# Performance work log

Measured on AMD Instinct MI355X. Metric: run time of the kernel, lower is better.

## Reference

```python
import jax, jax.numpy as jnp
import numpy as np

V = 50000   # vocab_size
D = 128     # emb_dim
HID = 64    # hidden_dim
HEADS = 4   # gat_heads
N = 20000   # n_nodes
E = 320000  # n_edges
SLOPE = 0.2 # PyG GATConv leaky_relu negative_slope


def setup_inputs() -> dict:
    key = jax.random.key(0)
    ks = jax.random.split(key, 13)
    nrm = lambda k, shp: jax.random.normal(k, shp, jnp.float32) * 0.1
    return {
        "node_idxs": jax.random.randint(ks[0], (N,), 0, V),
        "edge_index": jax.random.randint(ks[1], (2, E), 0, N),
        "emb": nrm(ks[2], (V, D)),
        # GAT layer 1: in=D, out=HID per head, HEADS heads, concat
        "W1": nrm(ks[3], (D, HEADS * HID)),
        "att_src1": nrm(ks[4], (HEADS, HID)),
        "att_dst1": nrm(ks[5], (HEADS, HID)),
        "b1": jnp.zeros((HEADS * HID,), jnp.float32),
        # GAT layer 2: in=HEADS*HID, out=HID, 1 head
        "W2": nrm(ks[6], (HEADS * HID, HID)),
        "att_src2": nrm(ks[7], (1, HID)),
        "att_dst2": nrm(ks[8], (1, HID)),
        "b2": jnp.zeros((HID,), jnp.float32),
        # attentional pooling gate MLP: Linear(HID,HID) -> ReLU -> Linear(HID,1)
        "gate_W1": nrm(ks[9], (HID, HID)),
        "gate_b1": jnp.zeros((HID,), jnp.float32),
        "gate_W2": nrm(ks[10], (HID, 1)),
        "gate_b2": jnp.zeros((1,), jnp.float32),
    }


def _segment_softmax(logits, seg, num_segments):
    # numerically stable softmax over edges grouped by destination node
    m = jax.ops.segment_max(logits, seg, num_segments=num_segments)
    e = jnp.exp(logits - m[seg])
    s = jax.ops.segment_sum(e, seg, num_segments=num_segments)
    return e / s[seg]


def _gat_layer(x, src, dst, n, W, a_src, a_dst, b, heads, ch):
    h = (x @ W).reshape(n, heads, ch)                 # [N,H,C]
    alpha_src = jnp.einsum('nhc,hc->nh', h, a_src)    # [N,H]
    alpha_dst = jnp.einsum('nhc,hc->nh', h, a_dst)    # [N,H]
    logits = jax.nn.leaky_relu(alpha_src[src] + alpha_dst[dst], SLOPE)  # [E,H]
    alpha = _segment_softmax(logits, dst, n)          # [E,H]
    out = jax.ops.segment_sum(h[src] * alpha[..., None], dst, num_segments=n)  # [N,H,C]
    return out.reshape(n, heads * ch) + b


def reference(node_idxs, edge_index, emb, W1, att_src1, att_dst1, b1,
              W2, att_src2, att_dst2, b2, gate_W1, gate_b1, gate_W2, gate_b2):
    n = node_idxs.shape[0]
    # PyG GATConv default add_self_loops=True
    loops = jnp.arange(n)
    src = jnp.concatenate([edge_index[0], loops])
    dst = jnp.concatenate([edge_index[1], loops])

    x = emb[node_idxs]                                                  # [N,D]
    x = jax.nn.elu(_gat_layer(x, src, dst, n, W1, att_src1, att_dst1, b1, HEADS, HID))
    x = jax.nn.elu(_gat_layer(x, src, dst, n, W2, att_src2, att_dst2, b2, 1, HID))

    # AttentionalAggregation with index=zeros -> global softmax-gated pool
    gate = jax.nn.relu(x @ gate_W1 + gate_b1) @ gate_W2 + gate_b2       # [N,1]
    w = jax.nn.softmax(gate, axis=0)
    return jnp.sum(w * x, axis=0, keepdims=True)                        # [1,HID]
```

## Files before the change

### kernel.cpp

```cpp
#include <hip/hip_runtime.h>

typedef float v4 __attribute__((ext_vector_type(4)));

__device__ __forceinline__ float leaky(float x) { return x >= 0.f ? x : 0.2f * x; }
__device__ __forceinline__ float elu(float x) { return x > 0.f ? x : expm1f(x); }

__global__ void k_deg(const int* __restrict__ ei, int* __restrict__ deg, int nE, int eT) {
  int e = blockIdx.x * blockDim.x + threadIdx.x;
  if (e >= eT) return;
  int d = (e < nE) ? ei[nE + e] : (e - nE);
  atomicAdd(&deg[d], 1);
}

__global__ void k_scan(const int* __restrict__ deg, int* __restrict__ rowptr,
                       int* __restrict__ cursor, int nN, int eT) {
  __shared__ int sd[1024];
  int t = threadIdx.x;
  int chunk = (nN + 1023) >> 10;
  int beg = t * chunk;
  int end = beg + chunk; if (end > nN) end = nN;
  int s = 0;
  for (int i = beg; i < end; ++i) s += deg[i];
  sd[t] = s;
  __syncthreads();
  for (int off = 1; off < 1024; off <<= 1) {
    int v = (t >= off) ? sd[t - off] : 0;
    __syncthreads();
    sd[t] += v;
    __syncthreads();
  }
  int run = sd[t] - s;
  for (int i = beg; i < end; ++i) { rowptr[i] = run; cursor[i] = run; run += deg[i]; }
  if (t == 0) rowptr[nN] = eT;
}

__global__ void k_scatter(const int* __restrict__ ei, int* __restrict__ cursor,
                          int* __restrict__ srt, int nE, int eT) {
  int e = blockIdx.x * blockDim.x + threadIdx.x;
  if (e >= eT) return;
  int s, d;
  if (e < nE) { s = ei[e]; d = ei[nE + e]; } else { s = d = e - nE; }
  int pos = atomicAdd(&cursor[d], 1);
  srt[pos] = s;
}

__global__ __launch_bounds__(256) void k_gemm1(
    const int* __restrict__ nidx, const float* __restrict__ emb,
    const float* __restrict__ W1, const float* __restrict__ asv,
    const float* __restrict__ adv, float* __restrict__ h1,
    float* __restrict__ as1, float* __restrict__ ad1, int nN) {
  __shared__ __align__(16) float xs[64 * 68];
  __shared__ __align__(16) float Ws[64 * 64];
  int t = threadIdx.x;
  int nbase = (blockIdx.x >> 2) * 64;
  int head  = blockIdx.x & 3;
  int cbase = head * 64;
  int c0 = (t & 15) * 4;
  int n0 = (t >> 4) * 4;
  float acc[4][4];
  for (int i = 0; i < 4; ++i) for (int j = 0; j < 4; ++j) acc[i][j] = 0.f;
  v4 z = (v4)(0.f);
  for (int kc = 0; kc < 2; ++kc) {
    __syncthreads();
    {
      int sn = t >> 2;
      int node = nbase + sn;
      int kp = (t & 3) * 16;
      bool v = node < nN;
      const float* sp = &emb[(size_t)nidx[v ? node : nN - 1] * 128 + kc * 64 + kp];
      v4 a0 = v ? *(const v4*)(sp + 0)  : z;
      v4 a1 = v ? *(const v4*)(sp + 4)  : z;
      v4 a2 = v ? *(const v4*)(sp + 8)  : z;
      v4 a3 = v ? *(const v4*)(sp + 12) : z;
      *(v4*)&xs[sn * 68 + kp + 0]  = a0;
      *(v4*)&xs[sn * 68 + kp + 4]  = a1;
      *(v4*)&xs[sn * 68 + kp + 8]  = a2;
      *(v4*)&xs[sn * 68 + kp + 12] = a3;
    }
    {
      int kk = t >> 2;
      int cp = (t & 3) * 16;
      const float* wp = &W1[(size_t)(kc * 64 + kk) * 256 + cbase + cp];
      v4 w0 = *(const v4*)(wp + 0);
      v4 w1 = *(const v4*)(wp + 4);
      v4 w2 = *(const v4*)(wp + 8);
      v4 w3 = *(const v4*)(wp + 12);
      *(v4*)&Ws[kk * 64 + cp + 0]  = w0;
      *(v4*)&Ws[kk * 64 + cp + 4]  = w1;
      *(v4*)&Ws[kk * 64 + cp + 8]  = w2;
      *(v4*)&Ws[kk * 64 + cp + 12] = w3;
    }
    __syncthreads();
    #pragma unroll 4
    for (int kk = 0; kk < 64; kk += 4) {
      v4 xv[4], wv[4];
      for (int i = 0; i < 4; ++i) xv[i] = *(const v4*)&xs[(n0 + i) * 68 + kk];
      for (int j = 0; j < 4; ++j) wv[j] = *(const v4*)&Ws[(kk + j) * 64 + c0];
      for (int i = 0; i < 4; ++i)
        for (int j = 0; j < 4; ++j) {
          float xd = xv[i][j];
          acc[i][0] += xd * wv[j][0];
          acc[i][1] += xd * wv[j][1];
          acc[i][2] += xd * wv[j][2];
          acc[i][3] += xd * wv[j][3];
        }
    }
  }
  v4 asl = *(const v4*)&asv[cbase + c0];
  v4 adl = *(const v4*)&adv[cbase + c0];
  for (int i = 0; i < 4; ++i) {
    int node = nbase + n0 + i;
    v4 o; o[0] = acc[i][0]; o[1] = acc[i][1]; o[2] = acc[i][2]; o[3] = acc[i][3];
    float ps = o[0]*asl[0] + o[1]*asl[1] + o[2]*asl[2] + o[3]*asl[3];
    float pd = o[0]*adl[0] + o[1]*adl[1] + o[2]*adl[2] + o[3]*adl[3];
    ps += __shfl_xor(ps, 1); pd += __shfl_xor(pd, 1);
    ps += __shfl_xor(ps, 2); pd += __shfl_xor(pd, 2);
    ps += __shfl_xor(ps, 4); pd += __shfl_xor(pd, 4);
    ps += __shfl_xor(ps, 8); pd += __shfl_xor(pd, 8);
    if (node < nN) {
      *(v4*)&h1[(size_t)node * 256 + cbase + c0] = o;
      if ((t & 15) == 0) {
        as1[(size_t)node * 4 + head] = ps;
        ad1[(size_t)node * 4 + head] = pd;
      }
    }
  }
}

__global__ __launch_bounds__(256) void k_agg1(
    const float* __restrict__ h1, const float* __restrict__ as1,
    const float* __restrict__ ad1, const float* __restrict__ b1,
    const int* __restrict__ rowptr, const int* __restrict__ srt,
    float* __restrict__ x2, int nN) {
  __shared__ int   ss[4][64];
  __shared__ float sw[4][256];
  int t = threadIdx.x;
  int wv = t >> 6, lane = t & 63;
  int n = blockIdx.x * 4 + wv;
  if (n >= nN) return;
  int ms0 = rowptr[n], ms1 = rowptr[n + 1];
  v4 adn = *(const v4*)&ad1[(size_t)n * 4];
  int h = lane >> 4;
  v4 acc = (v4)(0.f);
  float den = 0.f;
  for (int base = ms0; base < ms1; base += 64) {
    int m = ms1 - base; if (m > 64) m = 64;
    asm volatile("s_waitcnt lgkmcnt(0)" ::: "memory");
    __builtin_amdgcn_wave_barrier();
    if (lane < m) {
      int s = srt[base + lane];
      ss[wv][lane] = s;
      v4 a = *(const v4*)&as1[(size_t)s * 4];
      sw[wv][lane * 4 + 0] = __expf(leaky(a[0] + adn[0]));
      sw[wv][lane * 4 + 1] = __expf(leaky(a[1] + adn[1]));
      sw[wv][lane * 4 + 2] = __expf(leaky(a[2] + adn[2]));
      sw[wv][lane * 4 + 3] = __expf(leaky(a[3] + adn[3]));
    }
    asm volatile("s_waitcnt lgkmcnt(0)" ::: "memory");
    __builtin_amdgcn_wave_barrier();
    #pragma unroll 8
    for (int j = 0; j < m; ++j) {
      int s = ss[wv][j];
      float wj = sw[wv][j * 4 + h];
      v4 hv = *(const v4*)&h1[(size_t)s * 256 + lane * 4];
      acc[0] += wj * hv[0];
      acc[1] += wj * hv[1];
      acc[2] += wj * hv[2];
      acc[3] += wj * hv[3];
      den += wj;
    }
  }
  v4 bb = *(const v4*)&b1[lane * 4];
  float inv = 1.f / den;
  v4 o;
  o[0] = elu(acc[0] * inv + bb[0]);
  o[1] = elu(acc[1] * inv + bb[1]);
  o[2] = elu(acc[2] * inv + bb[2]);
  o[3] = elu(acc[3] * inv + bb[3]);
  *(v4*)&x2[(size_t)n * 256 + lane * 4] = o;
}

__global__ __launch_bounds__(256) void k_gemm2(
    const float* __restrict__ x2, const float* __restrict__ W2,
    const float* __restrict__ asv, const float* __restrict__ adv,
    float* __restrict__ h2, float* __restrict__ as2, float* __restrict__ ad2, int nN) {
  __shared__ __align__(16) float xs[32 * 68];
  __shared__ __align__(16) float Ws[64 * 64];
  int t = threadIdx.x;
  int nbase = blockIdx.x * 32;
  int c0 = (t & 15) * 4;
  int n0 = (t >> 4) * 2;
  float acc[2][4];
  for (int i = 0; i < 2; ++i) for (int j = 0; j < 4; ++j) acc[i][j] = 0.f;
  v4 z = (v4)(0.f);
  for (int kc = 0; kc < 4; ++kc) {
    __syncthreads();
    {
      int sn = t >> 3;
      int node = nbase + sn;
      int kp = (t & 7) * 8;
      bool v = node < nN;
      const float* sp = &x2[(size_t)(v ? node : nN - 1) * 256 + kc * 64 + kp];
      v4 a0 = v ? *(const v4*)(sp + 0) : z;
      v4 a1 = v ? *(const v4*)(sp + 4) : z;
      *(v4*)&xs[sn * 68 + kp + 0] = a0;
      *(v4*)&xs[sn * 68 + kp + 4] = a1;
    }
    {
      int kk = t >> 2;
      int cp = (t & 3) * 16;
      const float* wp = &W2[(size_t)(kc * 64 + kk) * 64 + cp];
      v4 w0 = *(const v4*)(wp + 0);
      v4 w1 = *(const v4*)(wp + 4);
      v4 w2 = *(const v4*)(wp + 8);
      v4 w3 = *(const v4*)(wp + 12);
      *(v4*)&Ws[kk * 64 + cp + 0]  = w0;
      *(v4*)&Ws[kk * 64 + cp + 4]  = w1;
      *(v4*)&Ws[kk * 64 + cp + 8]  = w2;
      *(v4*)&Ws[kk * 64 + cp + 12] = w3;
    }
    __syncthreads();
    #pragma unroll 4
    for (int kk = 0; kk < 64; kk += 4) {
      v4 xv[2], wv[4];
      for (int i = 0; i < 2; ++i) xv[i] = *(const v4*)&xs[(n0 + i) * 68 + kk];
      for (int j = 0; j < 4; ++j) wv[j] = *(const v4*)&Ws[(kk + j) * 64 + c0];
      for (int i = 0; i < 2; ++i)
        for (int j = 0; j < 4; ++j) {
          float xd = xv[i][j];
          acc[i][0] += xd * wv[j][0];
          acc[i][1] += xd * wv[j][1];
          acc[i][2] += xd * wv[j][2];
          acc[i][3] += xd * wv[j][3];
        }
    }
  }
  v4 asl = *(const v4*)&asv[c0];
  v4 adl = *(const v4*)&adv[c0];
  for (int i = 0; i < 2; ++i) {
    int node = nbase + n0 + i;
    v4 o; o[0] = acc[i][0]; o[1] = acc[i][1]; o[2] = acc[i][2]; o[3] = acc[i][3];
    float ps = o[0]*asl[0] + o[1]*asl[1] + o[2]*asl[2] + o[3]*asl[3];
    float pd = o[0]*adl[0] + o[1]*adl[1] + o[2]*adl[2] + o[3]*adl[3];
    ps += __shfl_xor(ps, 1); pd += __shfl_xor(pd, 1);
    ps += __shfl_xor(ps, 2); pd += __shfl_xor(pd, 2);
    ps += __shfl_xor(ps, 4); pd += __shfl_xor(pd, 4);
    ps += __shfl_xor(ps, 8); pd += __shfl_xor(pd, 8);
    if (node < nN) {
      *(v4*)&h2[(size_t)node * 64 + c0] = o;
      if ((t & 15) == 0) { as2[node] = ps; ad2[node] = pd; }
    }
  }
}

__global__ __launch_bounds__(256) void k_agg2(
    const float* __restrict__ h2, const float* __restrict__ as2,
    const float* __restrict__ ad2, const float* __restrict__ b2,
    const int* __restrict__ rowptr, const int* __restrict__ srt,
    float* __restrict__ x3, int nN) {
  __shared__ int   ss[4][64];
  __shared__ float sw[4][64];
  int t = threadIdx.x;
  int wv = t >> 6, lane = t & 63;
  int n = blockIdx.x * 4 + wv;
  if (n >= nN) return;
  int ms0 = rowptr[n], ms1 = rowptr[n + 1];
  float adn = ad2[n];
  float acc = 0.f, den = 0.f;
  for (int base = ms0; base < ms1; base += 64) {
    int m = ms1 - base; if (m > 64) m = 64;
    asm volatile("s_waitcnt lgkmcnt(0)" ::: "memory");
    __builtin_amdgcn_wave_barrier();
    if (lane < m) {
      int s = srt[base + lane];
      ss[wv][lane] = s;
      sw[wv][lane] = __expf(leaky(as2[s] + adn));
    }
    asm volatile("s_waitcnt lgkmcnt(0)" ::: "memory");
    __builtin_amdgcn_wave_barrier();
    #pragma unroll 8
    for (int j = 0; j < m; ++j) {
      int s = ss[wv][j];
      float wj = sw[wv][j];
      acc += wj * h2[(size_t)s * 64 + lane];
      den += wj;
    }
  }
  x3[(size_t)n * 64 + lane] = elu(acc / den + b2[lane]);
}

__global__ __launch_bounds__(512) void k_gatepool(
    const float* __restrict__ x3, const float* __restrict__ gW1,
    const float* __restrict__ gb1, const float* __restrict__ gW2,
    const float* __restrict__ gb2, float* __restrict__ pnum,
    float* __restrict__ pden, int nN) {
  __shared__ __align__(16) float gwT[64 * 68];
  __shared__ float xr[8][64];
  __shared__ float snum[8][64];
  __shared__ float sden[8];
  int t = threadIdx.x;
  int wv = t >> 6, lane = t & 63;
  for (int i = t; i < 4096; i += 512) {
    int d = i >> 6, c = i & 63;
    gwT[c * 68 + d] = gW1[i];
  }
  float gb1l = gb1[lane];
  float gw2l = gW2[lane];
  float gb2s = gb2[0];
  __syncthreads();
  float num = 0.f, den = 0.f;
  int nIt = (nN + 2047) >> 11;
  int off0 = blockIdx.x * 8 + wv;
  for (int it = 0; it < nIt; ++it) {
    int n = off0 + it * 2048;
    bool v = n < nN;
    float xv = v ? x3[(size_t)n * 64 + lane] : 0.f;
    xr[wv][lane] = xv;
    asm volatile("s_waitcnt lgkmcnt(0)" ::: "memory");
    __builtin_amdgcn_wave_barrier();
    float hid = gb1l;
    for (int d4 = 0; d4 < 64; d4 += 4) {
      v4 xs4 = *(const v4*)&xr[wv][d4];
      v4 gv  = *(const v4*)&gwT[lane * 68 + d4];
      hid += xs4[0] * gv[0] + xs4[1] * gv[1] + xs4[2] * gv[2] + xs4[3] * gv[3];
    }
    hid = fmaxf(hid, 0.f);
    float p = hid * gw2l;
    for (int o = 32; o; o >>= 1) p += __shfl_xor(p, o);
    float g = __expf(p + gb2s);
    if (v) { num += g * xv; den += g; }
    asm volatile("s_waitcnt lgkmcnt(0)" ::: "memory");
    __builtin_amdgcn_wave_barrier();
  }
  snum[wv][lane] = num;
  if (lane == 0) sden[wv] = den;
  __syncthreads();
  if (t < 64) {
    float s = 0.f;
    for (int k = 0; k < 8; ++k) s += snum[k][t];
    pnum[blockIdx.x * 64 + t] = s;
  }
  if (t == 0) {
    float s = 0.f;
    for (int k = 0; k < 8; ++k) s += sden[k];
    pden[blockIdx.x] = s;
  }
}

__global__ void k_final(const float* __restrict__ pnum, const float* __restrict__ pden,
                        float* __restrict__ out) {
  int t = threadIdx.x;
  float s = 0.f, dn = 0.f;
  for (int b = 0; b < 256; ++b) { s += pnum[b * 64 + t]; dn += pden[b]; }
  out[t] = s / dn;
}

extern "C" void kernel_launch(void* const* d_in, const int* in_sizes, int n_in,
                              void* d_out, int out_size, void* d_ws, size_t ws_size,
                              hipStream_t stream) {
  const int*   nidx = (const int*)d_in[0];
  const int*   ei   = (const int*)d_in[1];
  const float* emb  = (const float*)d_in[2];
  const float* W1   = (const float*)d_in[3];
  const float* as1v = (const float*)d_in[4];
  const float* ad1v = (const float*)d_in[5];
  const float* b1   = (const float*)d_in[6];
  const float* W2   = (const float*)d_in[7];
  const float* as2v = (const float*)d_in[8];
  const float* ad2v = (const float*)d_in[9];
  const float* b2   = (const float*)d_in[10];
  const float* gW1  = (const float*)d_in[11];
  const float* gb1  = (const float*)d_in[12];
  const float* gW2  = (const float*)d_in[13];
  const float* gb2  = (const float*)d_in[14];
  float* out = (float*)d_out;

  const int nN = in_sizes[0];
  const int nE = in_sizes[1] / 2;
  const int eT = nE + nN;

  float* f = (float*)d_ws;
  size_t off = 0;
  float* h1   = f + off; off += (size_t)nN * 256;
  float* x2   = f + off; off += (size_t)nN * 256;
  float* as1  = f + off; off += (size_t)nN * 4;
  float* ad1  = f + off; off += (size_t)nN * 4;
  float* as2  = f + off; off += nN;
  float* ad2  = f + off; off += nN;
  float* pnum = f + off; off += 256 * 64;
  float* pden = f + off; off += 256;
  int* deg    = (int*)(f + off); off += nN;
  int* rowptr = (int*)(f + off); off += nN + 1;
  int* cursor = (int*)(f + off); off += nN;
  int* srt    = (int*)(f + off); off += eT;

  float* h2 = h1;
  float* x3 = h1 + (size_t)nN * 128;

  hipMemsetAsync(deg, 0, (size_t)nN * sizeof(int), stream);

  int eb = (eT + 255) / 256;
  k_deg    <<<eb, 256, 0, stream>>>(ei, deg, nE, eT);
  k_scan   <<<1, 1024, 0, stream>>>(deg, rowptr, cursor, nN, eT);
  k_scatter<<<eb, 256, 0, stream>>>(ei, cursor, srt, nE, eT);

  int nt64 = (nN + 63) / 64;
  k_gemm1 <<<nt64 * 4, 256, 0, stream>>>(nidx, emb, W1, as1v, ad1v, h1, as1, ad1, nN);
  k_agg1  <<<(nN + 3) / 4, 256, 0, stream>>>(h1, as1, ad1, b1, rowptr, srt, x2, nN);

  k_gemm2 <<<(nN + 31) / 32, 256, 0, stream>>>(x2, W2, as2v, ad2v, h2, as2, ad2, nN);
  k_agg2  <<<(nN + 3) / 4, 256, 0, stream>>>(h2, as2, ad2, b2, rowptr, srt, x3, nN);

  k_gatepool<<<256, 512, 0, stream>>>(x3, gW1, gb1, gW2, gb2, pnum, pden, nN);
  k_final   <<<1, 64, 0, stream>>>(pnum, pden, out);
}
```

Baseline: 289.8 us.

## Fuse CSR build with GEMM1 tiles and fuse agg2 with gated pooling

The degree count and scan now run in one kernel alongside half of the GEMM1 tiles, with the last block doing the scan. The scatter runs in a second kernel alongside the other half of the tiles. Layer-2 aggregation is fused with the gate MLP and pooling, and the final division is done with atomics plus a last-block reduction. The goal is fewer launches, no x3 round trip through memory, and overlap of the graph preprocessing with GEMM work. In exchange it adds atomic float accumulation (nondeterministic order), a serial 256-thread scan, and a persistent tail grid of only 256 blocks, which may cut parallelism for the aggregation.

```diff
diff --git a/kernel.cpp b/kernel.cpp
--- a/kernel.cpp
+++ b/kernel.cpp
@@ -5,55 +5,16 @@
 __device__ __forceinline__ float leaky(float x) { return x >= 0.f ? x : 0.2f * x; }
 __device__ __forceinline__ float elu(float x) { return x > 0.f ? x : expm1f(x); }
 
-__global__ void k_deg(const int* __restrict__ ei, int* __restrict__ deg, int nE, int eT) {
-  int e = blockIdx.x * blockDim.x + threadIdx.x;
-  if (e >= eT) return;
-  int d = (e < nE) ? ei[nE + e] : (e - nE);
-  atomicAdd(&deg[d], 1);
-}
-
-__global__ void k_scan(const int* __restrict__ deg, int* __restrict__ rowptr,
-                       int* __restrict__ cursor, int nN, int eT) {
-  __shared__ int sd[1024];
-  int t = threadIdx.x;
-  int chunk = (nN + 1023) >> 10;
-  int beg = t * chunk;
-  int end = beg + chunk; if (end > nN) end = nN;
-  int s = 0;
-  for (int i = beg; i < end; ++i) s += deg[i];
-  sd[t] = s;
-  __syncthreads();
-  for (int off = 1; off < 1024; off <<= 1) {
-    int v = (t >= off) ? sd[t - off] : 0;
-    __syncthreads();
-    sd[t] += v;
-    __syncthreads();
-  }
-  int run = sd[t] - s;
-  for (int i = beg; i < end; ++i) { rowptr[i] = run; cursor[i] = run; run += deg[i]; }
-  if (t == 0) rowptr[nN] = eT;
-}
-
-__global__ void k_scatter(const int* __restrict__ ei, int* __restrict__ cursor,
-                          int* __restrict__ srt, int nE, int eT) {
-  int e = blockIdx.x * blockDim.x + threadIdx.x;
-  if (e >= eT) return;
-  int s, d;
-  if (e < nE) { s = ei[e]; d = ei[nE + e]; } else { s = d = e - nE; }
-  int pos = atomicAdd(&cursor[d], 1);
-  srt[pos] = s;
-}
-
-__global__ __launch_bounds__(256) void k_gemm1(
-    const int* __restrict__ nidx, const float* __restrict__ emb,
+__device__ __forceinline__ void gemm1_tile(
+    int tile, const int* __restrict__ nidx, const float* __restrict__ emb,
     const float* __restrict__ W1, const float* __restrict__ asv,
     const float* __restrict__ adv, float* __restrict__ h1,
-    float* __restrict__ as1, float* __restrict__ ad1, int nN) {
-  __shared__ __align__(16) float xs[64 * 68];
-  __shared__ __align__(16) float Ws[64 * 64];
-  int t = threadIdx.x;
-  int nbase = (blockIdx.x >> 2) * 64;
-  int head  = blockIdx.x & 3;
+    float* __restrict__ as1, float* __restrict__ ad1, int nN, float* smem) {
+  float* xs = smem;
+  float* Ws = smem + 64 * 68;
+  int t = threadIdx.x;
+  int nbase = (tile >> 2) * 64;
+  int head  = tile & 3;
   int cbase = head * 64;
   int c0 = (t & 15) * 4;
   int n0 = (t >> 4) * 4;
@@ -123,6 +84,80 @@
         as1[(size_t)node * 4 + head] = ps;
         ad1[(size_t)node * 4 + head] = pd;
       }
+    }
+  }
+}
+
+__global__ __launch_bounds__(256) void k_d2(
+    const int* __restrict__ nidx, const float* __restrict__ emb,
+    const float* __restrict__ W1, const float* __restrict__ asv,
+    const float* __restrict__ adv, float* __restrict__ h1,
+    float* __restrict__ as1, float* __restrict__ ad1,
+    const int* __restrict__ ei, int* __restrict__ deg,
+    int* __restrict__ rowptr, int* __restrict__ cursor, int* __restrict__ ctr2,
+    int nN, int nE, int eT, int g1, int ndeg) {
+  __shared__ __align__(16) float smem[64 * 68 + 64 * 64];
+  __shared__ int lastflag;
+  int b = blockIdx.x;
+  int t = threadIdx.x;
+  if (b < g1) { gemm1_tile(b, nidx, emb, W1, asv, adv, h1, as1, ad1, nN, smem); return; }
+  int bid = b - g1;
+  for (int r = 0; r < 4; ++r) {
+    int e = bid * 1024 + r * 256 + t;
+    if (e < eT) {
+      int d = (e < nE) ? ei[nE + e] : (e - nE);
+      atomicAdd(&deg[d], 1);
+    }
+  }
+  __syncthreads();
+  if (t == 0) {
+    __threadfence();
+    int old = atomicAdd(ctr2, 1);
+    lastflag = (old == ndeg - 1);
+  }
+  __syncthreads();
+  if (!lastflag) return;
+  int* sd = (int*)smem;
+  int chunk = (nN + 255) >> 8;
+  int beg = t * chunk;
+  int end = beg + chunk; if (end > nN) end = nN;
+  int s = 0;
+  for (int i = beg; i < end; ++i) s += atomicAdd(&deg[i], 0);
+  sd[t] = s;
+  __syncthreads();
+  for (int off = 1; off < 256; off <<= 1) {
+    int v = (t >= off) ? sd[t - off] : 0;
+    __syncthreads();
+    sd[t] += v;
+    __syncthreads();
+  }
+  int run = sd[t] - s;
+  for (int i = beg; i < end; ++i) {
+    int dv = atomicAdd(&deg[i], 0);
+    rowptr[i] = run; cursor[i] = run; run += dv;
+  }
+  if (t == 0) rowptr[nN] = eT;
+}
+
+__global__ __launch_bounds__(256) void k_d3(
+    const int* __restrict__ nidx, const float* __restrict__ emb,
+    const float* __restrict__ W1, const float* __restrict__ asv,
+    const float* __restrict__ adv, float* __restrict__ h1,
+    float* __restrict__ as1, float* __restrict__ ad1,
+    const int* __restrict__ ei, int* __restrict__ cursor, int* __restrict__ srt,
+    int nN, int nE, int eT, int g1) {
+  __shared__ __align__(16) float smem[64 * 68 + 64 * 64];
+  int b = blockIdx.x;
+  int t = threadIdx.x;
+  if (b < g1) { gemm1_tile(g1 + b, nidx, emb, W1, asv, adv, h1, as1, ad1, nN, smem); return; }
+  int bid = b - g1;
+  for (int r = 0; r < 4; ++r) {
+    int e = bid * 1024 + r * 256 + t;
+    if (e < eT) {
+      int s, d;
+      if (e < nE) { s = ei[e]; d = ei[nE + e]; } else { s = d = e - nE; }
+      int pos = atomicAdd(&cursor[d], 1);
+      srt[pos] = s;
     }
   }
 }
@@ -253,69 +288,57 @@
   }
 }
 
-__global__ __launch_bounds__(256) void k_agg2(
+__global__ __launch_bounds__(256) void k_tail(
     const float* __restrict__ h2, const float* __restrict__ as2,
     const float* __restrict__ ad2, const float* __restrict__ b2,
     const int* __restrict__ rowptr, const int* __restrict__ srt,
-    float* __restrict__ x3, int nN) {
+    const float* __restrict__ gW1, const float* __restrict__ gb1,
+    const float* __restrict__ gW2, const float* __restrict__ gb2,
+    float* __restrict__ pnum, float* __restrict__ pden, int* __restrict__ ctr3,
+    float* __restrict__ out, int nN) {
+  __shared__ __align__(16) float gwT[64 * 68];
   __shared__ int   ss[4][64];
   __shared__ float sw[4][64];
+  __shared__ float xr[4][64];
+  __shared__ float snum[4][64];
+  __shared__ float sden[4];
+  __shared__ int lastflag;
   int t = threadIdx.x;
   int wv = t >> 6, lane = t & 63;
-  int n = blockIdx.x * 4 + wv;
-  if (n >= nN) return;
-  int ms0 = rowptr[n], ms1 = rowptr[n + 1];
-  float adn = ad2[n];
-  float acc = 0.f, den = 0.f;
-  for (int base = ms0; base < ms1; base += 64) {
-    int m = ms1 - base; if (m > 64) m = 64;
+  for (int i = t; i < 4096; i += 256) {
+    int d = i >> 6, c = i & 63;
+    gwT[c * 68 + d] = gW1[i];
+  }
+  float gb1l = gb1[lane], gw2l = gW2[lane], gb2s = gb2[0], b2l = b2[lane];
+  __syncthreads();
+  float num = 0.f, denp = 0.f;
+  for (int n = blockIdx.x * 4 + wv; n < nN; n += 1024) {
+    int ms0 = rowptr[n], ms1 = rowptr[n + 1];
+    float adn = ad2[n];
+    float acc = 0.f, den = 0.f;
+    for (int base = ms0; base < ms1; base += 64) {
+      int m = ms1 - base; if (m > 64) m = 64;
+      asm volatile("s_waitcnt lgkmcnt(0)" ::: "memory");
+      __builtin_amdgcn_wave_barrier();
+      if (lane < m) {
+        int s = srt[base + lane];
+        ss[wv][lane] = s;
+        sw[wv][lane] = __expf(leaky(as2[s] + adn));
+      }
+      asm volatile("s_waitcnt lgkmcnt(0)" ::: "memory");
+      __builtin_amdgcn_wave_barrier();
+      #pragma unroll 8
+      for (int j = 0; j < m; ++j) {
+        int s = ss[wv][j];
+        float wj = sw[wv][j];
+        acc += wj * h2[(size_t)s * 64 + lane];
+        den += wj;
+      }
+    }
+    float x3v = elu(acc / den + b2l);
     asm volatile("s_waitcnt lgkmcnt(0)" ::: "memory");
     __builtin_amdgcn_wave_barrier();
-    if (lane < m) {
-      int s = srt[base + lane];
-      ss[wv][lane] = s;
-      sw[wv][lane] = __expf(leaky(as2[s] + adn));
-    }
-    asm volatile("s_waitcnt lgkmcnt(0)" ::: "memory");
-    __builtin_amdgcn_wave_barrier();
-    #pragma unroll 8
-    for (int j = 0; j < m; ++j) {
-      int s = ss[wv][j];
-      float wj = sw[wv][j];
-      acc += wj * h2[(size_t)s * 64 + lane];
-      den += wj;
-    }
-  }
-  x3[(size_t)n * 64 + lane] = elu(acc / den + b2[lane]);
-}
-
-__global__ __launch_bounds__(512) void k_gatepool(
-    const float* __restrict__ x3, const float* __restrict__ gW1,
-    const float* __restrict__ gb1, const float* __restrict__ gW2,
-    const float* __restrict__ gb2, float* __restrict__ pnum,
-    float* __restrict__ pden, int nN) {
-  __shared__ __align__(16) float gwT[64 * 68];
-  __shared__ float xr[8][64];
-  __shared__ float snum[8][64];
-  __shared__ float sden[8];
-  int t = threadIdx.x;
-  int wv = t >> 6, lane = t & 63;
-  for (int i = t; i < 4096; i += 512) {
-    int d = i >> 6, c = i & 63;
-    gwT[c * 68 + d] = gW1[i];
-  }
-  float gb1l = gb1[lane];
-  float gw2l = gW2[lane];
-  float gb2s = gb2[0];
-  __syncthreads();
-  float num = 0.f, den = 0.f;
-  int nIt = (nN + 2047) >> 11;
-  int off0 = blockIdx.x * 8 + wv;
-  for (int it = 0; it < nIt; ++it) {
-    int n = off0 + it * 2048;
-    bool v = n < nN;
-    float xv = v ? x3[(size_t)n * 64 + lane] : 0.f;
-    xr[wv][lane] = xv;
+    xr[wv][lane] = x3v;
     asm volatile("s_waitcnt lgkmcnt(0)" ::: "memory");
     __builtin_amdgcn_wave_barrier();
     float hid = gb1l;
@@ -328,31 +351,26 @@
     float p = hid * gw2l;
     for (int o = 32; o; o >>= 1) p += __shfl_xor(p, o);
     float g = __expf(p + gb2s);
-    if (v) { num += g * xv; den += g; }
-    asm volatile("s_waitcnt lgkmcnt(0)" ::: "memory");
-    __builtin_amdgcn_wave_barrier();
+    num += g * x3v;
+    denp += g;
   }
   snum[wv][lane] = num;
-  if (lane == 0) sden[wv] = den;
-  __syncthreads();
-  if (t < 64) {
-    float s = 0.f;
-    for (int k = 0; k < 8; ++k) s += snum[k][t];
-    pnum[blockIdx.x * 64 + t] = s;
-  }
+  if (lane == 0) sden[wv] = denp;
+  __syncthreads();
+  if (t < 64) atomicAdd(&pnum[t], snum[0][t] + snum[1][t] + snum[2][t] + snum[3][t]);
+  if (t == 0) atomicAdd(pden, sden[0] + sden[1] + sden[2] + sden[3]);
+  __syncthreads();
   if (t == 0) {
-    float s = 0.f;
-    for (int k = 0; k < 8; ++k) s += sden[k];
-    pden[blockIdx.x] = s;
-  }
-}
-
-__global__ void k_final(const float* __restrict__ pnum, const float* __restrict__ pden,
-                        float* __restrict__ out) {
-  int t = threadIdx.x;
-  float s = 0.f, dn = 0.f;
-  for (int b = 0; b < 256; ++b) { s += pnum[b * 64 + t]; dn += pden[b]; }
-  out[t] = s / dn;
+    __threadfence();
+    int old = atomicAdd(ctr3, 1);
+    lastflag = (old == (int)gridDim.x - 1);
+  }
+  __syncthreads();
+  if (lastflag && t < 64) {
+    float nv = atomicAdd(&pnum[t], 0.f);
+    float dv = atomicAdd(pden, 0.f);
+    out[t] = nv / dv;
+  }
 }
 
 extern "C" void kernel_launch(void* const* d_in, const int* in_sizes, int n_in,
@@ -387,30 +405,32 @@
   float* ad1  = f + off; off += (size_t)nN * 4;
   float* as2  = f + off; off += nN;
   float* ad2  = f + off; off += nN;
-  float* pnum = f + off; off += 256 * 64;
-  float* pden = f + off; off += 256;
-  int* deg    = (int*)(f + off); off += nN;
   int* rowptr = (int*)(f + off); off += nN + 1;
   int* cursor = (int*)(f + off); off += nN;
   int* srt    = (int*)(f + off); off += eT;
+  int*   deg  = (int*)(f + off); off += nN;
+  float* pnum = f + off; off += 64;
+  float* pden = f + off; off += 1;
+  int*   ctr2 = (int*)(f + off); off += 1;
+  int*   ctr3 = (int*)(f + off); off += 1;
 
   float* h2 = h1;
-  float* x3 = h1 + (size_t)nN * 128;
-
-  hipMemsetAsync(deg, 0, (size_t)nN * sizeof(int), stream);
-
-  int eb = (eT + 255) / 256;
-  k_deg    <<<eb, 256, 0, stream>>>(ei, deg, nE, eT);
-  k_scan   <<<1, 1024, 0, stream>>>(deg, rowptr, cursor, nN, eT);
-  k_scatter<<<eb, 256, 0, stream>>>(ei, cursor, srt, nE, eT);
+
+  hipMemsetAsync(deg, 0, (size_t)(nN + 67) * sizeof(int), stream);
 
   int nt64 = (nN + 63) / 64;
-  k_gemm1 <<<nt64 * 4, 256, 0, stream>>>(nidx, emb, W1, as1v, ad1v, h1, as1, ad1, nN);
-  k_agg1  <<<(nN + 3) / 4, 256, 0, stream>>>(h1, as1, ad1, b1, rowptr, srt, x2, nN);
-
-  k_gemm2 <<<(nN + 31) / 32, 256, 0, stream>>>(x2, W2, as2v, ad2v, h2, as2, ad2, nN);
-  k_agg2  <<<(nN + 3) / 4, 256, 0, stream>>>(h2, as2, ad2, b2, rowptr, srt, x3, nN);
-
-  k_gatepool<<<256, 512, 0, stream>>>(x3, gW1, gb1, gW2, gb2, pnum, pden, nN);
-  k_final   <<<1, 64, 0, stream>>>(pnum, pden, out);
-}
+  int g1   = (nt64 * 4 + 1) / 2;
+  int g1b  = nt64 * 4 - g1;
+  int ndeg = (eT + 1023) / 1024;
+
+  k_d2<<<g1 + ndeg, 256, 0, stream>>>(nidx, emb, W1, as1v, ad1v, h1, as1, ad1,
+                                      ei, deg, rowptr, cursor, ctr2,
+                                      nN, nE, eT, g1, ndeg);
+  k_d3<<<g1b + ndeg, 256, 0, stream>>>(nidx, emb, W1, as1v, ad1v, h1, as1, ad1,
+                                       ei, cursor, srt, nN, nE, eT, g1);
+
+  k_agg1 <<<(nN + 3) / 4, 256, 0, stream>>>(h1, as1, ad1, b1, rowptr, srt, x2, nN);
+  k_gemm2<<<(nN + 31) / 32, 256, 0, stream>>>(x2, W2, as2v, ad2v, h2, as2, ad2, nN);
+  k_tail <<<256, 256, 0, stream>>>(h2, as2, ad2, b2, rowptr, srt,
+                                   gW1, gb1, gW2, gb2, pnum, pden, ctr3, out, nN);
+}
```

After: 334.3 us. 15.3% more time.
